# Performance work log

Hardware: AMD Instinct MI355X
Metric: run time of the kernel (lower is better)

The kernel has to match this reference:

```python
import jax, jax.numpy as jnp
import numpy as np

B, D, C, F = 1024, 8192, 345, 512
PROTO_W = 0.99  # args.proto_m


def setup_inputs() -> dict:
    key = jax.random.key(0)
    k = jax.random.split(key, 6)
    img_q = jax.random.normal(k[0], (B, D), jnp.float32)
    img_q1 = jax.random.normal(k[1], (B, D), jnp.float32)
    # partial label mask: random candidate set, guarantee >=1 candidate per row
    partial_Y = (jax.random.uniform(k[2], (B, C)) < 0.3).astype(jnp.float32)
    partial_Y = partial_Y.at[jnp.arange(B), jnp.arange(B) % C].set(1.0)
    W_enc = jax.random.normal(k[3], (D, F), jnp.float32) / np.sqrt(D).astype(np.float32)
    W_fc = jax.random.normal(k[4], (F, C), jnp.float32) / np.sqrt(F).astype(np.float32)
    b_fc = jnp.zeros((C,), jnp.float32)
    proto = jax.random.normal(k[5], (C, F), jnp.float32)
    proto = proto / jnp.linalg.norm(proto, axis=1, keepdims=True)
    return {"img_q": img_q, "img_q1": img_q1, "partial_Y": partial_Y,
            "W_enc": W_enc, "W_fc": W_fc, "b_fc": b_fc, "proto": proto}


def reference(img_q, img_q1, partial_Y, W_enc, W_fc, b_fc, proto):
    # encoder: feats [B,F], logits [B,C] (abstracted backbone + shared fc)
    feats_q = img_q @ W_enc
    logits_q = feats_q @ W_fc + b_fc
    feats_q1 = img_q1 @ W_enc
    logits_q1 = feats_q1 @ W_fc + b_fc

    # partial-label restricted pseudo labels
    scores = jax.nn.softmax(logits_q, axis=1) * partial_Y
    scores = scores / scores.sum(axis=1, keepdims=True)
    labels = jnp.argmax(scores, axis=1)  # [B] int

    # Sequential per-sample EMA p[l] = w*p[l] + (1-w)*f, vectorized in closed form.
    # For a sample with c_after same-label samples occurring later, its final
    # contribution is (1-w)*w^c_after * f; the old prototype is scaled by w^count.
    onehot = jax.nn.one_hot(labels, C, dtype=feats_q.dtype)   # [B,C]
    cum = jnp.cumsum(onehot, axis=0)                          # inclusive counts
    occ = cum[jnp.arange(B), labels] - 1.0                    # occurrences before i
    total = cum[-1]                                           # [C] per-class counts
    c_after = total[labels] - occ - 1.0                       # [B]
    coef = (1.0 - PROTO_W) * PROTO_W ** c_after               # [B]
    contrib = jax.ops.segment_sum(coef[:, None] * feats_q, labels, num_segments=C)
    new_proto = (PROTO_W ** total)[:, None] * proto + contrib
    new_proto = new_proto / jnp.linalg.norm(new_proto, axis=1, keepdims=True)

    prot_scores = new_proto @ W_fc + b_fc
    return logits_q, logits_q1, new_proto, prot_scores, labels, feats_q, feats_q1
```

## Files before the change

kernel.cpp:

```cpp
#include <hip/hip_runtime.h>
#include <float.h>
#include <math.h>

#define B_SZ 1024
#define D_SZ 8192
#define C_SZ 345
#define F_SZ 512
#define PROTO_W 0.99f


#define WS_XH 0
#define WS_XL 33554432u
#define WS_WH 67108864u
#define WS_WL 75497472u
#define WS_P  83886080u
#define WS2_WFH 100663296u
#define WS2_WFL 101056512u
#define WS2_LAB 101449728u
#define WS2_NEED 101457920u
#define WS2_FH 0u
#define WS2_FL 2097152u

#define WS_NEED 92274688u
#define WS_FH  0u
#define WS_FL  2097152u
#define WS_WFH 4194304u
#define WS_WFL 4587520u
#define WS_NPH 4980736u
#define WS_NPL 5373952u

typedef short bf16x8 __attribute__((ext_vector_type(8)));
typedef short short4v __attribute__((ext_vector_type(4)));
typedef short short8v __attribute__((ext_vector_type(8)));
typedef float f32x4  __attribute__((ext_vector_type(4)));

__device__ __forceinline__ void split_bf16(float x, short& hi, short& lo) {
    unsigned u = __float_as_uint(x);
    unsigned r = (u + 0x7FFFu + ((u >> 16) & 1u)) >> 16;
    hi = (short)r;
    float hf = __uint_as_float(r << 16);
    lo = (short)(__float_as_uint(x - hf) >> 16);
}
__device__ __forceinline__ float bf16_f32(short h) {
    return __uint_as_float(((unsigned)(unsigned short)h) << 16);
}

__device__ __forceinline__ void gl_lds16(const short* g, short* l) {
    __builtin_amdgcn_global_load_lds(
        (const __attribute__((address_space(1))) void*)g,
        (__attribute__((address_space(3))) void*)l, 16, 0, 0);
}

__device__ __forceinline__ unsigned f2key(float v) {
    unsigned u = __float_as_uint(v);
    return (u & 0x80000000u) ? ~u : (u | 0x80000000u);
}

__device__ __forceinline__ void fence_barrier() {
    asm volatile("" ::: "memory");
    __builtin_amdgcn_s_barrier();
    asm volatile("" ::: "memory");
}

#define MFMA_BF16 __builtin_amdgcn_mfma_f32_16x16x32_bf16

#define MFMA_BLOCK(IA0, IA1, IB0, IB1)                                   \
    do {                                                                 \
        bf16x8 a0h = *(const bf16x8*)&sAh[IA0];                          \
        bf16x8 a1h = *(const bf16x8*)&sAh[IA1];                          \
        bf16x8 b0h = *(const bf16x8*)&sBh[IB0];                          \
        bf16x8 b1h = *(const bf16x8*)&sBh[IB1];                          \
        bf16x8 a0l = *(const bf16x8*)&sAl[IA0];                          \
        bf16x8 a1l = *(const bf16x8*)&sAl[IA1];                          \
        bf16x8 b0l = *(const bf16x8*)&sBl[IB0];                          \
        bf16x8 b1l = *(const bf16x8*)&sBl[IB1];                          \
        acc[0][0] = MFMA_BF16(a0h, b0h, acc[0][0], 0, 0, 0);             \
        acc[0][1] = MFMA_BF16(a0h, b1h, acc[0][1], 0, 0, 0);             \
        acc[1][0] = MFMA_BF16(a1h, b0h, acc[1][0], 0, 0, 0);             \
        acc[1][1] = MFMA_BF16(a1h, b1h, acc[1][1], 0, 0, 0);             \
        acc[0][0] = MFMA_BF16(a0h, b0l, acc[0][0], 0, 0, 0);             \
        acc[0][1] = MFMA_BF16(a0h, b1l, acc[0][1], 0, 0, 0);             \
        acc[1][0] = MFMA_BF16(a1h, b0l, acc[1][0], 0, 0, 0);             \
        acc[1][1] = MFMA_BF16(a1h, b1l, acc[1][1], 0, 0, 0);             \
        acc[0][0] = MFMA_BF16(a0l, b0h, acc[0][0], 0, 0, 0);             \
        acc[0][1] = MFMA_BF16(a0l, b1h, acc[0][1], 0, 0, 0);             \
        acc[1][0] = MFMA_BF16(a1l, b0h, acc[1][0], 0, 0, 0);             \
        acc[1][1] = MFMA_BF16(a1l, b1h, acc[1][1], 0, 0, 0);             \
    } while (0)

__global__ __launch_bounds__(256) void convert_all(
    const float* __restrict__ img_q, const float* __restrict__ img_q1,
    const float* __restrict__ W_enc, const float* __restrict__ W_fc,
    short* __restrict__ Xh, short* __restrict__ Xl,
    short* __restrict__ Wh, short* __restrict__ Wl,
    short* __restrict__ Wth, short* __restrict__ Wtl)
{
    __shared__ float tile[64][65];
    const int bid = blockIdx.x;
    const int t = threadIdx.x;

    if (bid < 1024) {
        const int HALF = (B_SZ * D_SZ) / 4;
        const int total = 2 * HALF;
        for (int i4 = bid * 256 + t; i4 < total; i4 += 1024 * 256) {
            float4 v = (i4 < HALF) ? ((const float4*)img_q)[i4]
                                   : ((const float4*)img_q1)[i4 - HALF];
            short4v h, l;
            short hh, ll;
            split_bf16(v.x, hh, ll); h.x = hh; l.x = ll;
            split_bf16(v.y, hh, ll); h.y = hh; l.y = ll;
            split_bf16(v.z, hh, ll); h.z = hh; l.z = ll;
            split_bf16(v.w, hh, ll); h.w = hh; l.w = ll;
            ((short4v*)Xh)[i4] = h;
            ((short4v*)Xl)[i4] = l;
        }
    } else if (bid < 2048) {
        const int id = bid - 1024;
        const int k0 = (id >> 3) * 64;
        const int n0 = (id & 7) * 64;
        {
            const int kr = t >> 2;
            const int cb = (t & 3) * 16;
#pragma unroll
            for (int j = 0; j < 4; ++j) {
                float4 v = *(const float4*)&W_enc[(size_t)(k0 + kr) * F_SZ + n0 + cb + j * 4];
                tile[kr][cb + j * 4 + 0] = v.x;
                tile[kr][cb + j * 4 + 1] = v.y;
                tile[kr][cb + j * 4 + 2] = v.z;
                tile[kr][cb + j * 4 + 3] = v.w;
            }
        }
        __syncthreads();
        const int n = t >> 2;
#pragma unroll
        for (int cc = 0; cc < 2; ++cc) {
            const int ch = (t & 3) * 2 + cc;
            short8v h, l;
#pragma unroll
            for (int e = 0; e < 8; ++e) {
                short hh, ll;
                split_bf16(tile[ch * 8 + e][n], hh, ll);
                h[e] = hh; l[e] = ll;
            }
            size_t off = (size_t)(n0 + n) * D_SZ + k0 + ch * 8;
            *(short8v*)&Wh[off] = h;
            *(short8v*)&Wl[off] = l;
        }
    } else {
        const int id = bid - 2048;
        const int k0 = (id & 7) * 64;
        const int c0 = (id >> 3) * 64;
        for (int idx = t; idx < 64 * 64; idx += 256) {
            const int kr = idx >> 6;
            const int cc = idx & 63;
            tile[kr][cc] = (c0 + cc < C_SZ) ? W_fc[(size_t)(k0 + kr) * C_SZ + c0 + cc] : 0.0f;
        }
        __syncthreads();
        const int crow = t >> 2;
#pragma unroll
        for (int cc2 = 0; cc2 < 2; ++cc2) {
            const int ch = (t & 3) * 2 + cc2;
            short8v h, l;
#pragma unroll
            for (int e = 0; e < 8; ++e) {
                short hh, ll;
                split_bf16(tile[ch * 8 + e][crow], hh, ll);
                h[e] = hh; l[e] = ll;
            }
            size_t off = (size_t)(c0 + crow) * F_SZ + k0 + ch * 8;
            *(short8v*)&Wth[off] = h;
            *(short8v*)&Wtl[off] = l;
        }
    }
}

__global__ __launch_bounds__(512, 1) void gemm_ws128_v3(
    const short* __restrict__ Xh, const short* __restrict__ Xl,
    const short* __restrict__ Wh, const short* __restrict__ Wl,
    float* __restrict__ P, int ksteps)
{
    __shared__ __align__(16) short sAh[2][8192];
    __shared__ __align__(16) short sAl[2][8192];
    __shared__ __align__(16) short sBh[2][8192];
    __shared__ __align__(16) short sBl[2][8192];

    const int t = threadIdx.x;
    const int lane = t & 63;
    const int wave = t >> 6;

    const int flat = blockIdx.x + 4 * blockIdx.y + 64 * blockIdx.z;
    const int logical = (flat & 7) * 32 + (flat >> 3);
    const int nt = logical & 3;
    const int mt = (logical >> 2) & 15;
    const int ks = logical >> 6;

    const int m0 = mt * 128;
    const int n0 = nt * 128;
    const int kbase = ks * ksteps * 64;

    const int arr = wave >> 1;
    const int half = wave & 1;
    const short* gbase =
        (arr == 0) ? Xh + (size_t)m0 * D_SZ :
        (arr == 1) ? Xl + (size_t)m0 * D_SZ :
        (arr == 2) ? Wh + (size_t)n0 * D_SZ :
                     Wl + (size_t)n0 * D_SZ;
    short* lb[2];
    lb[0] = ((arr == 0) ? sAh[0] : (arr == 1) ? sAl[0] : (arr == 2) ? sBh[0] : sBl[0]) + half * 4096;
    lb[1] = ((arr == 0) ? sAh[1] : (arr == 1) ? sAl[1] : (arr == 2) ? sBh[1] : sBl[1]) + half * 4096;
    const int lrow8 = lane >> 3;
    const int gchunkOff = ((lane & 7) ^ lrow8) * 8;
    const short* gsrc = gbase + (size_t)(half * 64 + lrow8) * D_SZ + kbase + gchunkOff;

    const int wr = wave >> 2;
    const int wc = wave & 3;
    const int mo = wr * 64;
    const int no = wc * 32;
    const int lr = lane & 15;
    const int lkg = lane >> 4;
    const int x7 = lr & 7;
    const int sl0 = lkg ^ x7;
    const int sl1 = (4 + lkg) ^ x7;
    int aoff[4], boff[2];
#pragma unroll
    for (int f = 0; f < 4; ++f) aoff[f] = (mo + 16 * f + lr) * 64;
#pragma unroll
    for (int g = 0; g < 2; ++g) boff[g] = (no + 16 * g + lr) * 64;

    f32x4 acc[4][2] = {};

#pragma unroll
    for (int j = 0; j < 8; ++j)
        gl_lds16(gsrc + (size_t)(8 * j) * D_SZ, lb[0] + j * 512);

    int buf = 0;
    for (int s = 0; s < ksteps; ++s) {
        if (s + 1 < ksteps) {
            short* dst = lb[buf ^ 1];
            const short* g = gsrc + (s + 1) * 64;
#pragma unroll
            for (int j = 0; j < 8; ++j)
                gl_lds16(g + (size_t)(8 * j) * D_SZ, dst + j * 512);
            asm volatile("s_waitcnt vmcnt(8)" ::: "memory");
        } else {
            asm volatile("s_waitcnt vmcnt(0)" ::: "memory");
        }
        fence_barrier();

        const short* pAh = sAh[buf];
        const short* pAl = sAl[buf];
        const short* pBh = sBh[buf];
        const short* pBl = sBl[buf];

        {
            bf16x8 ah[4], al[4], bh[2], bl_[2];
#pragma unroll
            for (int f = 0; f < 4; ++f) {
                ah[f] = *(const bf16x8*)&pAh[aoff[f] + sl0 * 8];
                al[f] = *(const bf16x8*)&pAl[aoff[f] + sl0 * 8];
            }
#pragma unroll
            for (int g = 0; g < 2; ++g) {
                bh[g]  = *(const bf16x8*)&pBh[boff[g] + sl0 * 8];
                bl_[g] = *(const bf16x8*)&pBl[boff[g] + sl0 * 8];
            }
            __builtin_amdgcn_s_setprio(1);
#pragma unroll
            for (int f = 0; f < 4; ++f)
#pragma unroll
                for (int g = 0; g < 2; ++g)
                    acc[f][g] = MFMA_BF16(ah[f], bh[g], acc[f][g], 0, 0, 0);
#pragma unroll
            for (int f = 0; f < 4; ++f)
#pragma unroll
                for (int g = 0; g < 2; ++g)
                    acc[f][g] = MFMA_BF16(ah[f], bl_[g], acc[f][g], 0, 0, 0);
#pragma unroll
            for (int f = 0; f < 4; ++f)
#pragma unroll
                for (int g = 0; g < 2; ++g)
                    acc[f][g] = MFMA_BF16(al[f], bh[g], acc[f][g], 0, 0, 0);
            __builtin_amdgcn_s_setprio(0);
        }
        fence_barrier();

        {
            bf16x8 ah[4], al[4], bh[2], bl_[2];
#pragma unroll
            for (int f = 0; f < 4; ++f) {
                ah[f] = *(const bf16x8*)&pAh[aoff[f] + sl1 * 8];
                al[f] = *(const bf16x8*)&pAl[aoff[f] + sl1 * 8];
            }
#pragma unroll
            for (int g = 0; g < 2; ++g) {
                bh[g]  = *(const bf16x8*)&pBh[boff[g] + sl1 * 8];
                bl_[g] = *(const bf16x8*)&pBl[boff[g] + sl1 * 8];
            }
            __builtin_amdgcn_s_setprio(1);
#pragma unroll
            for (int f = 0; f < 4; ++f)
#pragma unroll
                for (int g = 0; g < 2; ++g)
                    acc[f][g] = MFMA_BF16(ah[f], bh[g], acc[f][g], 0, 0, 0);
#pragma unroll
            for (int f = 0; f < 4; ++f)
#pragma unroll
                for (int g = 0; g < 2; ++g)
                    acc[f][g] = MFMA_BF16(ah[f], bl_[g], acc[f][g], 0, 0, 0);
#pragma unroll
            for (int f = 0; f < 4; ++f)
#pragma unroll
                for (int g = 0; g < 2; ++g)
                    acc[f][g] = MFMA_BF16(al[f], bh[g], acc[f][g], 0, 0, 0);
            __builtin_amdgcn_s_setprio(0);
        }
        fence_barrier();
        buf ^= 1;
    }

    float* Pout = P + (size_t)ks * (2048u * 512u);
#pragma unroll
    for (int f = 0; f < 4; ++f)
#pragma unroll
        for (int g = 0; g < 2; ++g) {
            const int col  = n0 + no + 16 * g + (lane & 15);
            const int row0 = m0 + mo + 16 * f + (lane >> 4) * 4;
#pragma unroll
            for (int r = 0; r < 4; ++r)
                Pout[(size_t)(row0 + r) * F_SZ + col] = acc[f][g][r];
        }
}

__global__ __launch_bounds__(256, 1) void gemm_ws128(
    const short* __restrict__ Xh, const short* __restrict__ Xl,
    const short* __restrict__ Wh, const short* __restrict__ Wl,
    float* __restrict__ P, int ksteps)
{
    __shared__ __align__(16) short sAh[2][8192];
    __shared__ __align__(16) short sAl[2][8192];
    __shared__ __align__(16) short sBh[2][8192];
    __shared__ __align__(16) short sBl[2][8192];

    const int t = threadIdx.x;
    const int lane = t & 63;
    const int wave = t >> 6;
    const int nt = blockIdx.x;
    const int mt = blockIdx.y;
    const int ks = blockIdx.z;
    const int m0 = mt * 128;
    const int n0 = nt * 128;
    const int kbase = ks * ksteps * 64;

    const short* gbase =
        (wave == 0) ? Xh + (size_t)m0 * D_SZ :
        (wave == 1) ? Xl + (size_t)m0 * D_SZ :
        (wave == 2) ? Wh + (size_t)n0 * D_SZ :
                      Wl + (size_t)n0 * D_SZ;
    short* lb[2];
    lb[0] = (wave == 0) ? sAh[0] : (wave == 1) ? sAl[0] : (wave == 2) ? sBh[0] : sBl[0];
    lb[1] = (wave == 0) ? sAh[1] : (wave == 1) ? sAl[1] : (wave == 2) ? sBh[1] : sBl[1];
    const int lrow8 = lane >> 3;
    const int gchunkOff = ((lane & 7) ^ lrow8) * 8;
    const short* gsrc = gbase + (size_t)lrow8 * D_SZ + kbase + gchunkOff;

    const int mo = (wave >> 1) * 64;
    const int no = (wave & 1) * 64;
    const int lr = lane & 15;
    const int lkg = lane >> 4;
    const int x7 = lr & 7;
    const int sl0 = lkg ^ x7;
    const int sl1 = (4 + lkg) ^ x7;
    int aoff[4], boff[4];
#pragma unroll
    for (int f = 0; f < 4; ++f) {
        aoff[f] = (mo + 16 * f + lr) * 64;
        boff[f] = (no + 16 * f + lr) * 64;
    }

    f32x4 acc[4][4] = {};

#pragma unroll
    for (int j = 0; j < 16; ++j)
        gl_lds16(gsrc + (size_t)(8 * j) * D_SZ, lb[0] + j * 512);

    int buf = 0;
    for (int s = 0; s < ksteps; ++s) {
        if (s + 1 < ksteps) {
            short* dst = lb[buf ^ 1];
            const short* g = gsrc + (s + 1) * 64;
#pragma unroll
            for (int j = 0; j < 16; ++j)
                gl_lds16(g + (size_t)(8 * j) * D_SZ, dst + j * 512);
            asm volatile("s_waitcnt vmcnt(16)" ::: "memory");
        } else {
            asm volatile("s_waitcnt vmcnt(0)" ::: "memory");
        }
        fence_barrier();

        __builtin_amdgcn_s_setprio(1);
        {
            const short* pAh = sAh[buf];
            const short* pAl = sAl[buf];
            const short* pBh = sBh[buf];
            const short* pBl = sBl[buf];
#pragma unroll
            for (int ksub = 0; ksub < 2; ++ksub) {
                const int sl = ksub ? sl1 : sl0;
                bf16x8 ah[4], al[4], bh[4], blo[4];
#pragma unroll
                for (int f = 0; f < 4; ++f) {
                    ah[f]  = *(const bf16x8*)&pAh[aoff[f] + sl * 8];
                    al[f]  = *(const bf16x8*)&pAl[aoff[f] + sl * 8];
                }
#pragma unroll
                for (int g = 0; g < 4; ++g) {
                    bh[g]  = *(const bf16x8*)&pBh[boff[g] + sl * 8];
                    blo[g] = *(const bf16x8*)&pBl[boff[g] + sl * 8];
                }
#pragma unroll
                for (int f = 0; f < 4; ++f)
#pragma unroll
                    for (int g = 0; g < 4; ++g)
                        acc[f][g] = MFMA_BF16(ah[f], bh[g], acc[f][g], 0, 0, 0);
#pragma unroll
                for (int f = 0; f < 4; ++f)
#pragma unroll
                    for (int g = 0; g < 4; ++g)
                        acc[f][g] = MFMA_BF16(ah[f], blo[g], acc[f][g], 0, 0, 0);
#pragma unroll
                for (int f = 0; f < 4; ++f)
#pragma unroll
                    for (int g = 0; g < 4; ++g)
                        acc[f][g] = MFMA_BF16(al[f], bh[g], acc[f][g], 0, 0, 0);
            }
        }
        __builtin_amdgcn_s_setprio(0);
        fence_barrier();
        buf ^= 1;
    }

    float* Pout = P + (size_t)ks * (2048u * 512u);
#pragma unroll
    for (int f = 0; f < 4; ++f)
#pragma unroll
        for (int g = 0; g < 4; ++g) {
            const int col  = n0 + no + 16 * g + (lane & 15);
            const int row0 = m0 + mo + 16 * f + (lane >> 4) * 4;
#pragma unroll
            for (int r = 0; r < 4; ++r)
                Pout[(size_t)(row0 + r) * F_SZ + col] = acc[f][g][r];
        }
}

__global__ __launch_bounds__(256) void reduce_feats4(
    const float* __restrict__ P, float* __restrict__ feats,
    short* __restrict__ Fh, short* __restrict__ Fl)
{
    const int i4 = blockIdx.x * 256 + threadIdx.x;
    float4 a = ((const float4*)P)[i4];
#pragma unroll
    for (int sl = 1; sl < 4; ++sl) {
        float4 b = ((const float4*)(P + (size_t)sl * (2048u * 512u)))[i4];
        a.x += b.x; a.y += b.y; a.z += b.z; a.w += b.w;
    }
    ((float4*)feats)[i4] = a;
    float v[4] = {a.x, a.y, a.z, a.w};
    short4v h, l;
    short hh, ll;
#pragma unroll
    for (int e = 0; e < 4; ++e) {
        split_bf16(v[e], hh, ll); h[e] = hh; l[e] = ll;
    }
    ((short4v*)Fh)[i4] = h;
    ((short4v*)Fl)[i4] = l;
}

__global__ __launch_bounds__(256, 2) void fc_logits3(
    const short* __restrict__ Ah, const short* __restrict__ Al,
    const short* __restrict__ Bh_g, const short* __restrict__ Bl_g,
    const float* __restrict__ bias, const float* __restrict__ partial_Y,
    float* __restrict__ logits, unsigned long long* __restrict__ labPack)
{
    __shared__ __align__(16) short dAh[2][4096];
    __shared__ __align__(16) short dAl[2][4096];
    __shared__ __align__(16) short dBh[2][4096];
    __shared__ __align__(16) short dBl[2][4096];

    const int t = threadIdx.x;
    const int lane = t & 63;
    const int wave = t >> 6;
    const int n0 = blockIdx.x * 64;
    const int m0 = blockIdx.y * 64;

    const int lrow8 = lane >> 3;
    const int colOff = ((lane & 7) ^ lrow8) * 8;

    const short* gsrc = (wave == 0) ? Ah : (wave == 1) ? Al
                      : (wave == 2) ? Bh_g : Bl_g;
    const int rbase = (wave < 2) ? m0 : n0;
    short* lb[2];
    lb[0] = (wave == 0) ? dAh[0] : (wave == 1) ? dAl[0] : (wave == 2) ? dBh[0] : dBl[0];
    lb[1] = (wave == 0) ? dAh[1] : (wave == 1) ? dAl[1] : (wave == 2) ? dBh[1] : dBl[1];
    const short* gbase = gsrc + (size_t)(rbase + lrow8) * F_SZ + colOff;

    const int mo = (wave >> 1) * 32;
    const int no = (wave & 1) * 32;
    const int lr = lane & 15;
    const int lkg = lane >> 4;
    const int x7 = lr & 7;
    const int sl0 = (0 + lkg) ^ x7;
    const int sl1 = (4 + lkg) ^ x7;
    const int ra0 = (mo + lr) * 64,      ra1 = (mo + 16 + lr) * 64;
    const int rb0 = (no + lr) * 64,      rb1 = (no + 16 + lr) * 64;
    const int a00 = ra0 + sl0 * 8, a01 = ra0 + sl1 * 8;
    const int a10 = ra1 + sl0 * 8, a11 = ra1 + sl1 * 8;
    const int b00 = rb0 + sl0 * 8, b01 = rb0 + sl1 * 8;
    const int b10 = rb1 + sl0 * 8, b11 = rb1 + sl1 * 8;

    f32x4 acc[2][2] = {};

#pragma unroll
    for (int j = 0; j < 8; ++j)
        gl_lds16(gbase + (size_t)(8 * j) * F_SZ, lb[0] + j * 512);

    int buf = 0;
    for (int s = 0; s < 8; ++s) {
        if (s + 1 < 8) {
            short* dst = lb[buf ^ 1];
            const short* g = gbase + (s + 1) * 64;
#pragma unroll
            for (int j = 0; j < 8; ++j)
                gl_lds16(g + (size_t)(8 * j) * F_SZ, dst + j * 512);
            asm volatile("s_waitcnt vmcnt(8)" ::: "memory");
        } else {
            asm volatile("s_waitcnt vmcnt(0)" ::: "memory");
        }
        fence_barrier();
        __builtin_amdgcn_s_setprio(1);
        {
            const short* sAh = dAh[buf];
            const short* sAl = dAl[buf];
            const short* sBh = dBh[buf];
            const short* sBl = dBl[buf];
            MFMA_BLOCK(a00, a10, b00, b10);
            MFMA_BLOCK(a01, a11, b01, b11);
        }
        __builtin_amdgcn_s_setprio(0);
        fence_barrier();
        buf ^= 1;
    }

    const bool doArg = (m0 < B_SZ);
#pragma unroll
    for (int f = 0; f < 2; ++f) {
#pragma unroll
        for (int r = 0; r < 4; ++r) {
            const int row = m0 + mo + f * 16 + (lane >> 4) * 4 + r;
            unsigned long long best = 0;
#pragma unroll
            for (int g = 0; g < 2; ++g) {
                const int col = n0 + no + g * 16 + (lane & 15);
                if (col < C_SZ) {
                    const float v = acc[f][g][r] + bias[col];
                    logits[(size_t)row * C_SZ + col] = v;
                    if (doArg && partial_Y[(size_t)row * C_SZ + col] != 0.0f) {
                        unsigned long long p = ((unsigned long long)f2key(v) << 32)
                                             | (unsigned long long)(0xFFFFFFFFu - (unsigned)col);
                        if (p > best) best = p;
                    }
                }
            }
            if (doArg) {
#pragma unroll
                for (int m = 1; m < 16; m <<= 1) {
                    unsigned long long o = __shfl_xor(best, m);
                    if (o > best) best = o;
                }
                if ((lane & 15) == 0 && best != 0)
                    atomicMax(&labPack[row], best);
            }
        }
    }
}

__global__ __launch_bounds__(512) void proto_scores_fused(
    const unsigned long long* __restrict__ labPack,
    const float* __restrict__ feats_q,
    const float* __restrict__ proto,
    const short* __restrict__ Wth, const short* __restrict__ Wtl,
    const float* __restrict__ b_fc,
    float* __restrict__ new_proto, float* __restrict__ scores,
    float* __restrict__ labels_f)
{
    __shared__ int rowlist[B_SZ];
    __shared__ int mcount_s;
    __shared__ float nprow[F_SZ];
    __shared__ float red[8];
    __shared__ float rinv_s;
    const int c = blockIdx.x;
    const int t = threadIdx.x;
    const int lane = t & 63;
    const int w = t >> 6;

    if (c == 0) {
#pragma unroll
        for (int j = 0; j < 2; ++j) {
            const int i = t + j * 512;
            int li = (int)(0xFFFFFFFFu - (unsigned)(labPack[i] & 0xFFFFFFFFull));
            labels_f[i] = (float)li;
        }
    }

    if (w == 0) {
        int k = 0;
#pragma unroll
        for (int ch = 0; ch < 16; ++ch) {
            unsigned long long pk = labPack[ch * 64 + lane];
            int li = (int)(0xFFFFFFFFu - (unsigned)(pk & 0xFFFFFFFFull));
            unsigned long long mask = __ballot(li == c);
            if (lane == 0) {
                while (mask) {
                    int p = __builtin_ctzll(mask);
                    mask &= mask - 1;
                    rowlist[k++] = ch * 64 + p;
                }
            }
            k = __shfl(k, 0);
        }
        if (lane == 0) mcount_s = k;
    }
    __syncthreads();
    const int m = mcount_s;

    float val = proto[(size_t)c * F_SZ + t];
    for (int k = 0; k < m; ++k)
        val = PROTO_W * val + (1.0f - PROTO_W) * feats_q[(size_t)rowlist[k] * F_SZ + t];

    float sq = val * val;
#pragma unroll
    for (int off = 32; off; off >>= 1) sq += __shfl_down(sq, off);
    if ((t & 63) == 0) red[t >> 6] = sq;
    __syncthreads();
    if (t == 0) {
        float s = 0.0f;
#pragma unroll
        for (int ww = 0; ww < 8; ++ww) s += red[ww];
        rinv_s = 1.0f / sqrtf(s);
    }
    __syncthreads();
    const float v = val * rinv_s;
    new_proto[(size_t)c * F_SZ + t] = v;
    nprow[t] = v;
    __syncthreads();

    float np8[8];
#pragma unroll
    for (int j = 0; j < 8; ++j) np8[j] = nprow[lane * 8 + j];
    for (int col = w; col < C_SZ; col += 8) {
        const short8v h = *(const short8v*)&Wth[(size_t)col * F_SZ + lane * 8];
        const short8v l = *(const short8v*)&Wtl[(size_t)col * F_SZ + lane * 8];
        float p = 0.0f;
#pragma unroll
        for (int j = 0; j < 8; ++j)
            p += np8[j] * (bf16_f32(h[j]) + bf16_f32(l[j]));
#pragma unroll
        for (int off = 32; off; off >>= 1) p += __shfl_down(p, off);
        if (lane == 0) scores[(size_t)c * C_SZ + col] = p + b_fc[col];
    }
}

__global__ __launch_bounds__(256) void reduce_feats_split(
    const float* __restrict__ P, float* __restrict__ feats,
    short* __restrict__ Fh, short* __restrict__ Fl,
    const float* __restrict__ W_fc,
    short* __restrict__ Wth, short* __restrict__ Wtl)
{
    const int bid = blockIdx.x;
    const int t = threadIdx.x;
    if (bid < 1024) {
        const int n4 = (2048 * 512) / 4;
        const float* P1 = P + 2048 * 512;
        for (int i4 = bid * 256 + t; i4 < n4; i4 += 1024 * 256) {
            float4 a = ((const float4*)P)[i4];
            float4 b = ((const float4*)P1)[i4];
            float v[4] = {a.x + b.x, a.y + b.y, a.z + b.z, a.w + b.w};
            short4v h, l;
            short hh, ll;
#pragma unroll
            for (int e = 0; e < 4; ++e) {
                feats[i4 * 4 + e] = v[e];
                split_bf16(v[e], hh, ll); h[e] = hh; l[e] = ll;
            }
            ((short4v*)Fh)[i4] = h;
            ((short4v*)Fl)[i4] = l;
        }
    } else {
        __shared__ float tile[64][65];
        const int id = bid - 1024;
        const int k0 = (id & 7) * 64;
        const int c0 = (id >> 3) * 64;
        for (int idx = t; idx < 64 * 64; idx += 256) {
            const int kr = idx >> 6;
            const int cc = idx & 63;
            tile[kr][cc] = (c0 + cc < C_SZ) ? W_fc[(size_t)(k0 + kr) * C_SZ + c0 + cc] : 0.0f;
        }
        __syncthreads();
        const int crow = t >> 2;
#pragma unroll
        for (int cc2 = 0; cc2 < 2; ++cc2) {
            const int ch = (t & 3) * 2 + cc2;
            short8v h, l;
#pragma unroll
            for (int e = 0; e < 8; ++e) {
                short hh, ll;
                split_bf16(tile[ch * 8 + e][crow], hh, ll);
                h[e] = hh; l[e] = ll;
            }
            size_t off = (size_t)(c0 + crow) * F_SZ + k0 + ch * 8;
            *(short8v*)&Wth[off] = h;
            *(short8v*)&Wtl[off] = l;
        }
    }
}

__global__ __launch_bounds__(256) void gemm_fc(
    const short* __restrict__ Ah, const short* __restrict__ Al,
    const short* __restrict__ Bh, const short* __restrict__ Bl,
    const float* __restrict__ bias, float* __restrict__ Cout, int M)
{
    __shared__ __align__(16) short sAh[4096];
    __shared__ __align__(16) short sAl[4096];
    __shared__ __align__(16) short sBh[4096];
    __shared__ __align__(16) short sBl[4096];

    const int t = threadIdx.x;
    const int lane = t & 63;
    const int wave = t >> 6;
    const int n0 = blockIdx.x * 64;
    const int m0 = blockIdx.y * 64;

    const int lrow8 = lane >> 3;
    const int colOff = ((lane & 7) ^ lrow8) * 8;

    short* lbase = (wave == 0) ? sAh : (wave == 1) ? sAl : (wave == 2) ? sBh : sBl;
    const short* gA = (wave == 1) ? Al : Ah;
    const short* gB = (wave == 3) ? Bl : Bh;
    const bool isA = wave < 2;

    const int mo = (wave >> 1) * 32;
    const int no = (wave & 1) * 32;
    const int lr = lane & 15;
    const int lkg = lane >> 4;
    const int x7 = lr & 7;
    const int sl0 = (0 + lkg) ^ x7;
    const int sl1 = (4 + lkg) ^ x7;
    const int ra0 = (mo + lr) * 64,      ra1 = (mo + 16 + lr) * 64;
    const int rb0 = (no + lr) * 64,      rb1 = (no + 16 + lr) * 64;
    const int a00 = ra0 + sl0 * 8, a01 = ra0 + sl1 * 8;
    const int a10 = ra1 + sl0 * 8, a11 = ra1 + sl1 * 8;
    const int b00 = rb0 + sl0 * 8, b01 = rb0 + sl1 * 8;
    const int b10 = rb1 + sl0 * 8, b11 = rb1 + sl1 * 8;

    f32x4 acc[2][2] = {};

    for (int s = 0; s < 8; ++s) {
        __syncthreads();
        if (isA) {
#pragma unroll
            for (int j = 0; j < 8; ++j) {
                int row = m0 + lrow8 + 8 * j;
                if (row > M - 1) row = M - 1;
                gl_lds16(gA + (size_t)row * F_SZ + s * 64 + colOff, lbase + j * 512);
            }
        } else {
#pragma unroll
            for (int j = 0; j < 8; ++j) {
                int row = n0 + lrow8 + 8 * j;
                gl_lds16(gB + (size_t)row * F_SZ + s * 64 + colOff, lbase + j * 512);
            }
        }
        __syncthreads();
        MFMA_BLOCK(a00, a10, b00, b10);
        MFMA_BLOCK(a01, a11, b01, b11);
    }

#pragma unroll
    for (int f = 0; f < 2; ++f)
#pragma unroll
        for (int g = 0; g < 2; ++g) {
            const int col  = n0 + no + g * 16 + (lane & 15);
            if (col >= C_SZ) continue;
            const float bb = bias[col];
            const int row0 = m0 + mo + f * 16 + (lane >> 4) * 4;
#pragma unroll
            for (int r = 0; r < 4; ++r) {
                const int row = row0 + r;
                if (row < M)
                    Cout[(size_t)row * C_SZ + col] = acc[f][g][r] + bb;
            }
        }
}

__global__ __launch_bounds__(64) void argmax_labels(
    const float* __restrict__ logits, const float* __restrict__ partial_Y,
    float* __restrict__ labels_f)
{
    const int i = blockIdx.x;
    const int lane = threadIdx.x;
    float best = -FLT_MAX;
    int bidx = C_SZ;
    for (int c = lane; c < C_SZ; c += 64) {
        if (partial_Y[(size_t)i * C_SZ + c] != 0.0f) {
            float v = logits[(size_t)i * C_SZ + c];
            if (v > best || (v == best && c < bidx)) { best = v; bidx = c; }
        }
    }
#pragma unroll
    for (int off = 32; off; off >>= 1) {
        float ov = __shfl_down(best, off);
        int oi = __shfl_down(bidx, off);
        if (ov > best || (ov == best && oi < bidx)) { best = ov; bidx = oi; }
    }
    if (lane == 0) labels_f[i] = (float)bidx;
}

__global__ __launch_bounds__(512) void proto_update(
    const float* __restrict__ labels_f, const float* __restrict__ feats_q,
    const float* __restrict__ proto, float* __restrict__ new_proto,
    short* __restrict__ NPh, short* __restrict__ NPl)
{
    __shared__ int lab[B_SZ];
    __shared__ float red[8];
    __shared__ float rinv_s;
    const int c = blockIdx.x;
    const int t = threadIdx.x;
    for (int i = t; i < B_SZ; i += 512) lab[i] = (int)labels_f[i];
    __syncthreads();
    float val = proto[(size_t)c * F_SZ + t];
    for (int i = 0; i < B_SZ; ++i) {
        if (lab[i] == c)
            val = PROTO_W * val + (1.0f - PROTO_W) * feats_q[(size_t)i * F_SZ + t];
    }
    float sq = val * val;
#pragma unroll
    for (int off = 32; off; off >>= 1) sq += __shfl_down(sq, off);
    if ((t & 63) == 0) red[t >> 6] = sq;
    __syncthreads();
    if (t == 0) {
        float s = 0.0f;
#pragma unroll
        for (int w = 0; w < 8; ++w) s += red[w];
        rinv_s = 1.0f / sqrtf(s);
    }
    __syncthreads();
    const float v = val * rinv_s;
    new_proto[(size_t)c * F_SZ + t] = v;
    if (NPh) {
        short hh, ll;
        split_bf16(v, hh, ll);
        NPh[(size_t)c * F_SZ + t] = hh;
        NPl[(size_t)c * F_SZ + t] = ll;
    }
}

extern "C" void kernel_launch(void* const* d_in, const int* in_sizes, int n_in,
                              void* d_out, int out_size, void* d_ws, size_t ws_size,
                              hipStream_t stream)
{
    const float* img_q     = (const float*)d_in[0];
    const float* img_q1    = (const float*)d_in[1];
    const float* partial_Y = (const float*)d_in[2];
    const float* W_enc     = (const float*)d_in[3];
    const float* W_fc      = (const float*)d_in[4];
    const float* b_fc      = (const float*)d_in[5];
    const float* proto     = (const float*)d_in[6];

    float* out       = (float*)d_out;
    float* logits    = out;
    float* new_proto = out + 706560;
    float* scores    = out + 883200;
    float* labels_f  = out + 1002225;
    float* feats     = out + 1003249;

    char* ws = (char*)d_ws;
    short* Xh = (short*)(ws + WS_XH);
    short* Xl = (short*)(ws + WS_XL);
    short* Wh = (short*)(ws + WS_WH);
    short* Wl = (short*)(ws + WS_WL);
    float* P  = (float*)(ws + WS_P);

    if (ws_size >= (size_t)WS2_NEED) {
        short* Wth = (short*)(ws + WS2_WFH);
        short* Wtl = (short*)(ws + WS2_WFL);
        unsigned long long* labPack = (unsigned long long*)(ws + WS2_LAB);
        short* Fh = (short*)(ws + WS2_FH);
        short* Fl = (short*)(ws + WS2_FL);

        hipMemsetAsync(labPack, 0, B_SZ * sizeof(unsigned long long), stream);
        hipLaunchKernelGGL(convert_all, dim3(2096), dim3(256), 0, stream,
                           img_q, img_q1, W_enc, W_fc, Xh, Xl, Wh, Wl, Wth, Wtl);
        hipLaunchKernelGGL(gemm_ws128_v3, dim3(4, 16, 4), dim3(512), 0, stream,
                           Xh, Xl, Wh, Wl, P, 32);
        hipLaunchKernelGGL(reduce_feats4, dim3(1024), dim3(256), 0, stream,
                           P, feats, Fh, Fl);
        hipLaunchKernelGGL(fc_logits3, dim3(6, 32), dim3(256), 0, stream,
                           Fh, Fl, Wth, Wtl, b_fc, partial_Y, logits, labPack);
        hipLaunchKernelGGL(proto_scores_fused, dim3(345), dim3(512), 0, stream,
                           labPack, feats, proto, Wth, Wtl, b_fc,
                           new_proto, scores, labels_f);
    } else {
        short* Fh  = (short*)(ws + WS_FH);
        short* Fl  = (short*)(ws + WS_FL);
        short* Wth = (short*)(ws + WS_WFH);
        short* Wtl = (short*)(ws + WS_WFL);
        short* NPh = (short*)(ws + WS_NPH);
        short* NPl = (short*)(ws + WS_NPL);

        hipLaunchKernelGGL(convert_all, dim3(2048), dim3(256), 0, stream,
                           img_q, img_q1, W_enc, W_fc, Xh, Xl, Wh, Wl,
                           (short*)nullptr, (short*)nullptr);
        hipLaunchKernelGGL(gemm_ws128, dim3(4, 16, 2), dim3(256), 0, stream,
                           Xh, Xl, Wh, Wl, P, 64);
        hipLaunchKernelGGL(reduce_feats_split, dim3(1072), dim3(256), 0, stream,
                           P, feats, Fh, Fl, W_fc, Wth, Wtl);
        hipLaunchKernelGGL(gemm_fc, dim3(6, 32), dim3(256), 0, stream,
                           Fh, Fl, Wth, Wtl, b_fc, logits, 2048);
        hipLaunchKernelGGL(argmax_labels, dim3(1024), dim3(64), 0, stream,
                           logits, partial_Y, labels_f);
        hipLaunchKernelGGL(proto_update, dim3(345), dim3(512), 0, stream,
                           labels_f, feats, proto, new_proto, NPh, NPl);
        hipLaunchKernelGGL(gemm_fc, dim3(6, 6), dim3(256), 0, stream,
                           NPh, NPl, Wth, Wtl, b_fc, scores, C_SZ);
    }
}
```

Measured before the change: 248.2 us.

## Pre-pack bf16 split operands into tile-contiguous swizzled layout for GEMM

The conversion kernel now writes the hi/lo bf16 splits of the inputs and the encoder weight into a per-tile, per-kstep packed layout that already matches the swizzled LDS layout. This lets the main GEMM load each k-step as one contiguous 16 KB chunk instead of strided rows. The labPack clear is folded into the conversion kernel, which drops a separate memset launch. The cost is a more scattered write pattern during conversion, including a transposed store path for W_enc.

```diff
diff --git a/kernel.cpp b/kernel.cpp
--- a/kernel.cpp
+++ b/kernel.cpp
@@ -18,8 +18,6 @@
 #define WS2_WFL 101056512u
 #define WS2_LAB 101449728u
 #define WS2_NEED 101457920u
-#define WS2_FH 0u
-#define WS2_FL 2097152u
 
 #define WS_NEED 92274688u
 #define WS_FH  0u
@@ -88,16 +86,505 @@
         acc[1][1] = MFMA_BF16(a1l, b1h, acc[1][1], 0, 0, 0);             \
     } while (0)
 
+__device__ __forceinline__ int packed_off(int r, int c) {
+    const int half = r >> 6;
+    const int rh = r & 63;
+    const int j = rh >> 3;
+    const int r8 = rh & 7;
+    const int l = (r8 << 3) | (c ^ r8);
+    return half * 4096 + j * 512 + l * 8;
+}
+
+__global__ __launch_bounds__(256) void convert_pack(
+    const float* __restrict__ img_q, const float* __restrict__ img_q1,
+    const float* __restrict__ W_enc, const float* __restrict__ W_fc,
+    short* __restrict__ Ahp, short* __restrict__ Alp,
+    short* __restrict__ Bhp, short* __restrict__ Blp,
+    short* __restrict__ Wth, short* __restrict__ Wtl,
+    unsigned long long* __restrict__ labPack)
+{
+    __shared__ float tile[64][65];
+    const int bid = blockIdx.x;
+    const int t = threadIdx.x;
+
+    if (bid < 4)
+        labPack[bid * 256 + t] = 0ull;
+
+    if (bid < 1024) {
+        const int total = 2048 * 1024;
+        for (int i = bid * 256 + t; i < total; i += 1024 * 256) {
+            const int row = i >> 10;
+            const int cc = i & 1023;
+            const float* src = (row < B_SZ)
+                ? &img_q[(size_t)row * D_SZ + cc * 8]
+                : &img_q1[(size_t)(row - B_SZ) * D_SZ + cc * 8];
+            float4 a = ((const float4*)src)[0];
+            float4 b = ((const float4*)src)[1];
+            float f[8] = {a.x, a.y, a.z, a.w, b.x, b.y, b.z, b.w};
+            short8v h, l;
+#pragma unroll
+            for (int e = 0; e < 8; ++e) {
+                short hh, ll;
+                split_bf16(f[e], hh, ll);
+                h[e] = hh; l[e] = ll;
+            }
+            const int mt = row >> 7;
+            const int pr = row & 127;
+            const int kstep = cc >> 3;
+            const int c = cc & 7;
+            const size_t dst = (size_t)(mt * 128 + kstep) * 8192 + packed_off(pr, c);
+            *(short8v*)&Ahp[dst] = h;
+            *(short8v*)&Alp[dst] = l;
+        }
+    } else if (bid < 2048) {
+        const int id = bid - 1024;
+        const int kstep = id >> 3;
+        const int k0 = kstep * 64;
+        const int n0 = (id & 7) * 64;
+        {
+            const int kr = t >> 2;
+            const int cb = (t & 3) * 16;
+#pragma unroll
+            for (int j = 0; j < 4; ++j) {
+                float4 v = *(const float4*)&W_enc[(size_t)(k0 + kr) * F_SZ + n0 + cb + j * 4];
+                tile[kr][cb + j * 4 + 0] = v.x;
+                tile[kr][cb + j * 4 + 1] = v.y;
+                tile[kr][cb + j * 4 + 2] = v.z;
+                tile[kr][cb + j * 4 + 3] = v.w;
+            }
+        }
+        __syncthreads();
+        const int n = t >> 2;
+#pragma unroll
+        for (int cc2 = 0; cc2 < 2; ++cc2) {
+            const int ch = (t & 3) * 2 + cc2;
+            short8v h, l;
+#pragma unroll
+            for (int e = 0; e < 8; ++e) {
+                short hh, ll;
+                split_bf16(tile[ch * 8 + e][n], hh, ll);
+                h[e] = hh; l[e] = ll;
+            }
+            const int nrow = n0 + n;
+            const int nt = nrow >> 7;
+            const int pr = nrow & 127;
+            const size_t dst = (size_t)(nt * 128 + kstep) * 8192 + packed_off(pr, ch);
+            *(short8v*)&Bhp[dst] = h;
+            *(short8v*)&Blp[dst] = l;
+        }
+    } else {
+        const int id = bid - 2048;
+        const int k0 = (id & 7) * 64;
+        const int c0 = (id >> 3) * 64;
+        for (int idx = t; idx < 64 * 64; idx += 256) {
+            const int kr = idx >> 6;
+            const int cc = idx & 63;
+            tile[kr][cc] = (c0 + cc < C_SZ) ? W_fc[(size_t)(k0 + kr) * C_SZ + c0 + cc] : 0.0f;
+        }
+        __syncthreads();
+        const int crow = t >> 2;
+#pragma unroll
+        for (int cc2 = 0; cc2 < 2; ++cc2) {
+            const int ch = (t & 3) * 2 + cc2;
+            short8v h, l;
+#pragma unroll
+            for (int e = 0; e < 8; ++e) {
+                short hh, ll;
+                split_bf16(tile[ch * 8 + e][crow], hh, ll);
+                h[e] = hh; l[e] = ll;
+            }
+            size_t off = (size_t)(c0 + crow) * F_SZ + k0 + ch * 8;
+            *(short8v*)&Wth[off] = h;
+            *(short8v*)&Wtl[off] = l;
+        }
+    }
+}
+
+__global__ __launch_bounds__(512, 1) void gemm_ws128_v4(
+    const short* __restrict__ Ahp, const short* __restrict__ Alp,
+    const short* __restrict__ Bhp, const short* __restrict__ Blp,
+    float* __restrict__ P, int ksteps)
+{
+    __shared__ __align__(16) short sAh[2][8192];
+    __shared__ __align__(16) short sAl[2][8192];
+    __shared__ __align__(16) short sBh[2][8192];
+    __shared__ __align__(16) short sBl[2][8192];
+
+    const int t = threadIdx.x;
+    const int lane = t & 63;
+    const int wave = t >> 6;
+
+    const int flat = blockIdx.x + 4 * blockIdx.y + 64 * blockIdx.z;
+    const int logical = (flat & 7) * 32 + (flat >> 3);
+    const int nt = logical & 3;
+    const int mt = (logical >> 2) & 15;
+    const int ks = logical >> 6;
+
+    const int m0 = mt * 128;
+    const int n0 = nt * 128;
+
+    const int arr = wave >> 1;
+    const int half = wave & 1;
+    const short* gtile =
+        (arr == 0) ? Ahp + (size_t)(mt * 128) * 8192 :
+        (arr == 1) ? Alp + (size_t)(mt * 128) * 8192 :
+        (arr == 2) ? Bhp + (size_t)(nt * 128) * 8192 :
+                     Blp + (size_t)(nt * 128) * 8192;
+    short* lb[2];
+    lb[0] = ((arr == 0) ? sAh[0] : (arr == 1) ? sAl[0] : (arr == 2) ? sBh[0] : sBl[0]) + half * 4096;
+    lb[1] = ((arr == 0) ? sAh[1] : (arr == 1) ? sAl[1] : (arr == 2) ? sBh[1] : sBl[1]) + half * 4096;
+    const short* gsrc0 = gtile + (size_t)(ks * ksteps) * 8192 + half * 4096 + lane * 8;
+
+    const int wr = wave >> 2;
+    const int wc = wave & 3;
+    const int mo = wr * 64;
+    const int no = wc * 32;
+    const int lr = lane & 15;
+    const int lkg = lane >> 4;
+    const int x7 = lr & 7;
+    const int sl0 = lkg ^ x7;
+    const int sl1 = (4 + lkg) ^ x7;
+    int aoff[4], boff[2];
+#pragma unroll
+    for (int f = 0; f < 4; ++f) aoff[f] = (mo + 16 * f + lr) * 64;
+#pragma unroll
+    for (int g = 0; g < 2; ++g) boff[g] = (no + 16 * g + lr) * 64;
+
+    f32x4 acc[4][2] = {};
+
+#pragma unroll
+    for (int j = 0; j < 8; ++j)
+        gl_lds16(gsrc0 + j * 512, lb[0] + j * 512);
+
+    int buf = 0;
+    for (int s = 0; s < ksteps; ++s) {
+        if (s + 1 < ksteps) {
+            short* dst = lb[buf ^ 1];
+            const short* g = gsrc0 + (size_t)(s + 1) * 8192;
+#pragma unroll
+            for (int j = 0; j < 8; ++j)
+                gl_lds16(g + j * 512, dst + j * 512);
+            asm volatile("s_waitcnt vmcnt(8)" ::: "memory");
+        } else {
+            asm volatile("s_waitcnt vmcnt(0)" ::: "memory");
+        }
+        fence_barrier();
+
+        const short* pAh = sAh[buf];
+        const short* pAl = sAl[buf];
+        const short* pBh = sBh[buf];
+        const short* pBl = sBl[buf];
+
+        {
+            bf16x8 ah[4], al[4], bh[2], bl_[2];
+#pragma unroll
+            for (int f = 0; f < 4; ++f) {
+                ah[f] = *(const bf16x8*)&pAh[aoff[f] + sl0 * 8];
+                al[f] = *(const bf16x8*)&pAl[aoff[f] + sl0 * 8];
+            }
+#pragma unroll
+            for (int g = 0; g < 2; ++g) {
+                bh[g]  = *(const bf16x8*)&pBh[boff[g] + sl0 * 8];
+                bl_[g] = *(const bf16x8*)&pBl[boff[g] + sl0 * 8];
+            }
+            __builtin_amdgcn_s_setprio(1);
+#pragma unroll
+            for (int f = 0; f < 4; ++f)
+#pragma unroll
+                for (int g = 0; g < 2; ++g)
+                    acc[f][g] = MFMA_BF16(ah[f], bh[g], acc[f][g], 0, 0, 0);
+#pragma unroll
+            for (int f = 0; f < 4; ++f)
+#pragma unroll
+                for (int g = 0; g < 2; ++g)
+                    acc[f][g] = MFMA_BF16(ah[f], bl_[g], acc[f][g], 0, 0, 0);
+#pragma unroll
+            for (int f = 0; f < 4; ++f)
+#pragma unroll
+                for (int g = 0; g < 2; ++g)
+                    acc[f][g] = MFMA_BF16(al[f], bh[g], acc[f][g], 0, 0, 0);
+            __builtin_amdgcn_s_setprio(0);
+        }
+        fence_barrier();
+
+        {
+            bf16x8 ah[4], al[4], bh[2], bl_[2];
+#pragma unroll
+            for (int f = 0; f < 4; ++f) {
+                ah[f] = *(const bf16x8*)&pAh[aoff[f] + sl1 * 8];
+                al[f] = *(const bf16x8*)&pAl[aoff[f] + sl1 * 8];
+            }
+#pragma unroll
+            for (int g = 0; g < 2; ++g) {
+                bh[g]  = *(const bf16x8*)&pBh[boff[g] + sl1 * 8];
+                bl_[g] = *(const bf16x8*)&pBl[boff[g] + sl1 * 8];
+            }
+            __builtin_amdgcn_s_setprio(1);
+#pragma unroll
+            for (int f = 0; f < 4; ++f)
+#pragma unroll
+                for (int g = 0; g < 2; ++g)
+                    acc[f][g] = MFMA_BF16(ah[f], bh[g], acc[f][g], 0, 0, 0);
+#pragma unroll
+            for (int f = 0; f < 4; ++f)
+#pragma unroll
+                for (int g = 0; g < 2; ++g)
+                    acc[f][g] = MFMA_BF16(ah[f], bl_[g], acc[f][g], 0, 0, 0);
+#pragma unroll
+            for (int f = 0; f < 4; ++f)
+#pragma unroll
+                for (int g = 0; g < 2; ++g)
+                    acc[f][g] = MFMA_BF16(al[f], bh[g], acc[f][g], 0, 0, 0);
+            __builtin_amdgcn_s_setprio(0);
+        }
+        fence_barrier();
+        buf ^= 1;
+    }
+
+    float* Pout = P + (size_t)ks * (2048u * 512u);
+#pragma unroll
+    for (int f = 0; f < 4; ++f)
+#pragma unroll
+        for (int g = 0; g < 2; ++g) {
+            const int col  = n0 + no + 16 * g + (lane & 15);
+            const int row0 = m0 + mo + 16 * f + (lane >> 4) * 4;
+#pragma unroll
+            for (int r = 0; r < 4; ++r)
+                Pout[(size_t)(row0 + r) * F_SZ + col] = acc[f][g][r];
+        }
+}
+
+__global__ __launch_bounds__(256) void reduce_feats4(
+    const float* __restrict__ P, float* __restrict__ feats,
+    short* __restrict__ Fh, short* __restrict__ Fl)
+{
+    const int i4 = blockIdx.x * 256 + threadIdx.x;
+    float4 a = ((const float4*)P)[i4];
+#pragma unroll
+    for (int sl = 1; sl < 4; ++sl) {
+        float4 b = ((const float4*)(P + (size_t)sl * (2048u * 512u)))[i4];
+        a.x += b.x; a.y += b.y; a.z += b.z; a.w += b.w;
+    }
+    ((float4*)feats)[i4] = a;
+    float v[4] = {a.x, a.y, a.z, a.w};
+    short4v h, l;
+    short hh, ll;
+#pragma unroll
+    for (int e = 0; e < 4; ++e) {
+        split_bf16(v[e], hh, ll); h[e] = hh; l[e] = ll;
+    }
+    ((short4v*)Fh)[i4] = h;
+    ((short4v*)Fl)[i4] = l;
+}
+
+__global__ __launch_bounds__(256, 2) void fc_logits3(
+    const short* __restrict__ Ah, const short* __restrict__ Al,
+    const short* __restrict__ Bh_g, const short* __restrict__ Bl_g,
+    const float* __restrict__ bias, const float* __restrict__ partial_Y,
+    float* __restrict__ logits, unsigned long long* __restrict__ labPack)
+{
+    __shared__ __align__(16) short dAh[2][4096];
+    __shared__ __align__(16) short dAl[2][4096];
+    __shared__ __align__(16) short dBh[2][4096];
+    __shared__ __align__(16) short dBl[2][4096];
+
+    const int t = threadIdx.x;
+    const int lane = t & 63;
+    const int wave = t >> 6;
+    const int n0 = blockIdx.x * 64;
+    const int m0 = blockIdx.y * 64;
+
+    const int lrow8 = lane >> 3;
+    const int colOff = ((lane & 7) ^ lrow8) * 8;
+
+    const short* gsrc = (wave == 0) ? Ah : (wave == 1) ? Al
+                      : (wave == 2) ? Bh_g : Bl_g;
+    const int rbase = (wave < 2) ? m0 : n0;
+    short* lb[2];
+    lb[0] = (wave == 0) ? dAh[0] : (wave == 1) ? dAl[0] : (wave == 2) ? dBh[0] : dBl[0];
+    lb[1] = (wave == 0) ? dAh[1] : (wave == 1) ? dAl[1] : (wave == 2) ? dBh[1] : dBl[1];
+    const short* gbase = gsrc + (size_t)(rbase + lrow8) * F_SZ + colOff;
+
+    const int mo = (wave >> 1) * 32;
+    const int no = (wave & 1) * 32;
+    const int lr = lane & 15;
+    const int lkg = lane >> 4;
+    const int x7 = lr & 7;
+    const int sl0 = (0 + lkg) ^ x7;
+    const int sl1 = (4 + lkg) ^ x7;
+    const int ra0 = (mo + lr) * 64,      ra1 = (mo + 16 + lr) * 64;
+    const int rb0 = (no + lr) * 64,      rb1 = (no + 16 + lr) * 64;
+    const int a00 = ra0 + sl0 * 8, a01 = ra0 + sl1 * 8;
+    const int a10 = ra1 + sl0 * 8, a11 = ra1 + sl1 * 8;
+    const int b00 = rb0 + sl0 * 8, b01 = rb0 + sl1 * 8;
+    const int b10 = rb1 + sl0 * 8, b11 = rb1 + sl1 * 8;
+
+    f32x4 acc[2][2] = {};
+
+#pragma unroll
+    for (int j = 0; j < 8; ++j)
+        gl_lds16(gbase + (size_t)(8 * j) * F_SZ, lb[0] + j * 512);
+
+    int buf = 0;
+    for (int s = 0; s < 8; ++s) {
+        if (s + 1 < 8) {
+            short* dst = lb[buf ^ 1];
+            const short* g = gbase + (s + 1) * 64;
+#pragma unroll
+            for (int j = 0; j < 8; ++j)
+                gl_lds16(g + (size_t)(8 * j) * F_SZ, dst + j * 512);
+            asm volatile("s_waitcnt vmcnt(8)" ::: "memory");
+        } else {
+            asm volatile("s_waitcnt vmcnt(0)" ::: "memory");
+        }
+        fence_barrier();
+        __builtin_amdgcn_s_setprio(1);
+        {
+            const short* sAh = dAh[buf];
+            const short* sAl = dAl[buf];
+            const short* sBh = dBh[buf];
+            const short* sBl = dBl[buf];
+            MFMA_BLOCK(a00, a10, b00, b10);
+            MFMA_BLOCK(a01, a11, b01, b11);
+        }
+        __builtin_amdgcn_s_setprio(0);
+        fence_barrier();
+        buf ^= 1;
+    }
+
+    const bool doArg = (m0 < B_SZ);
+#pragma unroll
+    for (int f = 0; f < 2; ++f) {
+#pragma unroll
+        for (int r = 0; r < 4; ++r) {
+            const int row = m0 + mo + f * 16 + (lane >> 4) * 4 + r;
+            unsigned long long best = 0;
+#pragma unroll
+            for (int g = 0; g < 2; ++g) {
+                const int col = n0 + no + g * 16 + (lane & 15);
+                if (col < C_SZ) {
+                    const float v = acc[f][g][r] + bias[col];
+                    logits[(size_t)row * C_SZ + col] = v;
+                    if (doArg && partial_Y[(size_t)row * C_SZ + col] != 0.0f) {
+                        unsigned long long p = ((unsigned long long)f2key(v) << 32)
+                                             | (unsigned long long)(0xFFFFFFFFu - (unsigned)col);
+                        if (p > best) best = p;
+                    }
+                }
+            }
+            if (doArg) {
+#pragma unroll
+                for (int m = 1; m < 16; m <<= 1) {
+                    unsigned long long o = __shfl_xor(best, m);
+                    if (o > best) best = o;
+                }
+                if ((lane & 15) == 0 && best != 0)
+                    atomicMax(&labPack[row], best);
+            }
+        }
+    }
+}
+
+__global__ __launch_bounds__(512) void proto_scores_fused(
+    const unsigned long long* __restrict__ labPack,
+    const float* __restrict__ feats_q,
+    const float* __restrict__ proto,
+    const short* __restrict__ Wth, const short* __restrict__ Wtl,
+    const float* __restrict__ b_fc,
+    float* __restrict__ new_proto, float* __restrict__ scores,
+    float* __restrict__ labels_f)
+{
+    __shared__ int rowlist[B_SZ];
+    __shared__ int mcount_s;
+    __shared__ float nprow[F_SZ];
+    __shared__ float red[8];
+    __shared__ float rinv_s;
+    const int c = blockIdx.x;
+    const int t = threadIdx.x;
+    const int lane = t & 63;
+    const int w = t >> 6;
+
+    if (c == 0) {
+#pragma unroll
+        for (int j = 0; j < 2; ++j) {
+            const int i = t + j * 512;
+            int li = (int)(0xFFFFFFFFu - (unsigned)(labPack[i] & 0xFFFFFFFFull));
+            labels_f[i] = (float)li;
+        }
+    }
+
+    if (w == 0) {
+        int k = 0;
+#pragma unroll
+        for (int ch = 0; ch < 16; ++ch) {
+            unsigned long long pk = labPack[ch * 64 + lane];
+            int li = (int)(0xFFFFFFFFu - (unsigned)(pk & 0xFFFFFFFFull));
+            unsigned long long mask = __ballot(li == c);
+            if (lane == 0) {
+                while (mask) {
+                    int p = __builtin_ctzll(mask);
+                    mask &= mask - 1;
+                    rowlist[k++] = ch * 64 + p;
+                }
+            }
+            k = __shfl(k, 0);
+        }
+        if (lane == 0) mcount_s = k;
+    }
+    __syncthreads();
+    const int m = mcount_s;
+
+    float val = proto[(size_t)c * F_SZ + t];
+    for (int k = 0; k < m; ++k)
+        val = PROTO_W * val + (1.0f - PROTO_W) * feats_q[(size_t)rowlist[k] * F_SZ + t];
+
+    float sq = val * val;
+#pragma unroll
+    for (int off = 32; off; off >>= 1) sq += __shfl_down(sq, off);
+    if ((t & 63) == 0) red[t >> 6] = sq;
+    __syncthreads();
+    if (t == 0) {
+        float s = 0.0f;
+#pragma unroll
+        for (int ww = 0; ww < 8; ++ww) s += red[ww];
+        rinv_s = 1.0f / sqrtf(s);
+    }
+    __syncthreads();
+    const float v = val * rinv_s;
+    new_proto[(size_t)c * F_SZ + t] = v;
+    nprow[t] = v;
+    __syncthreads();
+
+    float np8[8];
+#pragma unroll
+    for (int j = 0; j < 8; ++j) np8[j] = nprow[lane * 8 + j];
+    for (int col = w; col < C_SZ; col += 8) {
+        const short8v h = *(const short8v*)&Wth[(size_t)col * F_SZ + lane * 8];
+        const short8v l = *(const short8v*)&Wtl[(size_t)col * F_SZ + lane * 8];
+        float p = 0.0f;
+#pragma unroll
+        for (int j = 0; j < 8; ++j)
+            p += np8[j] * (bf16_f32(h[j]) + bf16_f32(l[j]));
+#pragma unroll
+        for (int off = 32; off; off >>= 1) p += __shfl_down(p, off);
+        if (lane == 0) scores[(size_t)c * C_SZ + col] = p + b_fc[col];
+    }
+}
+
 __global__ __launch_bounds__(256) void convert_all(
     const float* __restrict__ img_q, const float* __restrict__ img_q1,
     const float* __restrict__ W_enc, const float* __restrict__ W_fc,
     short* __restrict__ Xh, short* __restrict__ Xl,
     short* __restrict__ Wh, short* __restrict__ Wl,
-    short* __restrict__ Wth, short* __restrict__ Wtl)
+    short* __restrict__ Wth, short* __restrict__ Wtl,
+    unsigned long long* __restrict__ labPack)
 {
     __shared__ float tile[64][65];
     const int bid = blockIdx.x;
     const int t = threadIdx.x;
+
+    if (labPack && bid < 4)
+        labPack[bid * 256 + t] = 0ull;
 
     if (bid < 1024) {
         const int HALF = (B_SZ * D_SZ) / 4;
@@ -174,163 +661,6 @@
     }
 }
 
-__global__ __launch_bounds__(512, 1) void gemm_ws128_v3(
-    const short* __restrict__ Xh, const short* __restrict__ Xl,
-    const short* __restrict__ Wh, const short* __restrict__ Wl,
-    float* __restrict__ P, int ksteps)
-{
-    __shared__ __align__(16) short sAh[2][8192];
-    __shared__ __align__(16) short sAl[2][8192];
-    __shared__ __align__(16) short sBh[2][8192];
-    __shared__ __align__(16) short sBl[2][8192];
-
-    const int t = threadIdx.x;
-    const int lane = t & 63;
-    const int wave = t >> 6;
-
-    const int flat = blockIdx.x + 4 * blockIdx.y + 64 * blockIdx.z;
-    const int logical = (flat & 7) * 32 + (flat >> 3);
-    const int nt = logical & 3;
-    const int mt = (logical >> 2) & 15;
-    const int ks = logical >> 6;
-
-    const int m0 = mt * 128;
-    const int n0 = nt * 128;
-    const int kbase = ks * ksteps * 64;
-
-    const int arr = wave >> 1;
-    const int half = wave & 1;
-    const short* gbase =
-        (arr == 0) ? Xh + (size_t)m0 * D_SZ :
-        (arr == 1) ? Xl + (size_t)m0 * D_SZ :
-        (arr == 2) ? Wh + (size_t)n0 * D_SZ :
-                     Wl + (size_t)n0 * D_SZ;
-    short* lb[2];
-    lb[0] = ((arr == 0) ? sAh[0] : (arr == 1) ? sAl[0] : (arr == 2) ? sBh[0] : sBl[0]) + half * 4096;
-    lb[1] = ((arr == 0) ? sAh[1] : (arr == 1) ? sAl[1] : (arr == 2) ? sBh[1] : sBl[1]) + half * 4096;
-    const int lrow8 = lane >> 3;
-    const int gchunkOff = ((lane & 7) ^ lrow8) * 8;
-    const short* gsrc = gbase + (size_t)(half * 64 + lrow8) * D_SZ + kbase + gchunkOff;
-
-    const int wr = wave >> 2;
-    const int wc = wave & 3;
-    const int mo = wr * 64;
-    const int no = wc * 32;
-    const int lr = lane & 15;
-    const int lkg = lane >> 4;
-    const int x7 = lr & 7;
-    const int sl0 = lkg ^ x7;
-    const int sl1 = (4 + lkg) ^ x7;
-    int aoff[4], boff[2];
-#pragma unroll
-    for (int f = 0; f < 4; ++f) aoff[f] = (mo + 16 * f + lr) * 64;
-#pragma unroll
-    for (int g = 0; g < 2; ++g) boff[g] = (no + 16 * g + lr) * 64;
-
-    f32x4 acc[4][2] = {};
-
-#pragma unroll
-    for (int j = 0; j < 8; ++j)
-        gl_lds16(gsrc + (size_t)(8 * j) * D_SZ, lb[0] + j * 512);
-
-    int buf = 0;
-    for (int s = 0; s < ksteps; ++s) {
-        if (s + 1 < ksteps) {
-            short* dst = lb[buf ^ 1];
-            const short* g = gsrc + (s + 1) * 64;
-#pragma unroll
-            for (int j = 0; j < 8; ++j)
-                gl_lds16(g + (size_t)(8 * j) * D_SZ, dst + j * 512);
-            asm volatile("s_waitcnt vmcnt(8)" ::: "memory");
-        } else {
-            asm volatile("s_waitcnt vmcnt(0)" ::: "memory");
-        }
-        fence_barrier();
-
-        const short* pAh = sAh[buf];
-        const short* pAl = sAl[buf];
-        const short* pBh = sBh[buf];
-        const short* pBl = sBl[buf];
-
-        {
-            bf16x8 ah[4], al[4], bh[2], bl_[2];
-#pragma unroll
-            for (int f = 0; f < 4; ++f) {
-                ah[f] = *(const bf16x8*)&pAh[aoff[f] + sl0 * 8];
-                al[f] = *(const bf16x8*)&pAl[aoff[f] + sl0 * 8];
-            }
-#pragma unroll
-            for (int g = 0; g < 2; ++g) {
-                bh[g]  = *(const bf16x8*)&pBh[boff[g] + sl0 * 8];
-                bl_[g] = *(const bf16x8*)&pBl[boff[g] + sl0 * 8];
-            }
-            __builtin_amdgcn_s_setprio(1);
-#pragma unroll
-            for (int f = 0; f < 4; ++f)
-#pragma unroll
-                for (int g = 0; g < 2; ++g)
-                    acc[f][g] = MFMA_BF16(ah[f], bh[g], acc[f][g], 0, 0, 0);
-#pragma unroll
-            for (int f = 0; f < 4; ++f)
-#pragma unroll
-                for (int g = 0; g < 2; ++g)
-                    acc[f][g] = MFMA_BF16(ah[f], bl_[g], acc[f][g], 0, 0, 0);
-#pragma unroll
-            for (int f = 0; f < 4; ++f)
-#pragma unroll
-                for (int g = 0; g < 2; ++g)
-                    acc[f][g] = MFMA_BF16(al[f], bh[g], acc[f][g], 0, 0, 0);
-            __builtin_amdgcn_s_setprio(0);
-        }
-        fence_barrier();
-
-        {
-            bf16x8 ah[4], al[4], bh[2], bl_[2];
-#pragma unroll
-            for (int f = 0; f < 4; ++f) {
-                ah[f] = *(const bf16x8*)&pAh[aoff[f] + sl1 * 8];
-                al[f] = *(const bf16x8*)&pAl[aoff[f] + sl1 * 8];
-            }
-#pragma unroll
-            for (int g = 0; g < 2; ++g) {
-                bh[g]  = *(const bf16x8*)&pBh[boff[g] + sl1 * 8];
-                bl_[g] = *(const bf16x8*)&pBl[boff[g] + sl1 * 8];
-            }
-            __builtin_amdgcn_s_setprio(1);
-#pragma unroll
-            for (int f = 0; f < 4; ++f)
-#pragma unroll
-                for (int g = 0; g < 2; ++g)
-                    acc[f][g] = MFMA_BF16(ah[f], bh[g], acc[f][g], 0, 0, 0);
-#pragma unroll
-            for (int f = 0; f < 4; ++f)
-#pragma unroll
-                for (int g = 0; g < 2; ++g)
-                    acc[f][g] = MFMA_BF16(ah[f], bl_[g], acc[f][g], 0, 0, 0);
-#pragma unroll
-            for (int f = 0; f < 4; ++f)
-#pragma unroll
-                for (int g = 0; g < 2; ++g)
-                    acc[f][g] = MFMA_BF16(al[f], bh[g], acc[f][g], 0, 0, 0);
-            __builtin_amdgcn_s_setprio(0);
-        }
-        fence_barrier();
-        buf ^= 1;
-    }
-
-    float* Pout = P + (size_t)ks * (2048u * 512u);
-#pragma unroll
-    for (int f = 0; f < 4; ++f)
-#pragma unroll
-        for (int g = 0; g < 2; ++g) {
-            const int col  = n0 + no + 16 * g + (lane & 15);
-            const int row0 = m0 + mo + 16 * f + (lane >> 4) * 4;
-#pragma unroll
-            for (int r = 0; r < 4; ++r)
-                Pout[(size_t)(row0 + r) * F_SZ + col] = acc[f][g][r];
-        }
-}
-
 __global__ __launch_bounds__(256, 1) void gemm_ws128(
     const short* __restrict__ Xh, const short* __restrict__ Xl,
     const short* __restrict__ Wh, const short* __restrict__ Wl,
@@ -452,39 +782,69 @@
         }
 }
 
-__global__ __launch_bounds__(256) void reduce_feats4(
+__global__ __launch_bounds__(256) void reduce_feats_split(
     const float* __restrict__ P, float* __restrict__ feats,
-    short* __restrict__ Fh, short* __restrict__ Fl)
-{
-    const int i4 = blockIdx.x * 256 + threadIdx.x;
-    float4 a = ((const float4*)P)[i4];
-#pragma unroll
-    for (int sl = 1; sl < 4; ++sl) {
-        float4 b = ((const float4*)(P + (size_t)sl * (2048u * 512u)))[i4];
-        a.x += b.x; a.y += b.y; a.z += b.z; a.w += b.w;
-    }
-    ((float4*)feats)[i4] = a;
-    float v[4] = {a.x, a.y, a.z, a.w};
-    short4v h, l;
-    short hh, ll;
-#pragma unroll
-    for (int e = 0; e < 4; ++e) {
-        split_bf16(v[e], hh, ll); h[e] = hh; l[e] = ll;
-    }
-    ((short4v*)Fh)[i4] = h;
-    ((short4v*)Fl)[i4] = l;
-}
-
-__global__ __launch_bounds__(256, 2) void fc_logits3(
+    short* __restrict__ Fh, short* __restrict__ Fl,
+    const float* __restrict__ W_fc,
+    short* __restrict__ Wth, short* __restrict__ Wtl)
+{
+    const int bid = blockIdx.x;
+    const int t = threadIdx.x;
+    if (bid < 1024) {
+        const int n4 = (2048 * 512) / 4;
+        const float* P1 = P + 2048 * 512;
+        for (int i4 = bid * 256 + t; i4 < n4; i4 += 1024 * 256) {
+            float4 a = ((const float4*)P)[i4];
+            float4 b = ((const float4*)P1)[i4];
+            float v[4] = {a.x + b.x, a.y + b.y, a.z + b.z, a.w + b.w};
+            short4v h, l;
+            short hh, ll;
+#pragma unroll
+            for (int e = 0; e < 4; ++e) {
+                feats[i4 * 4 + e] = v[e];
+                split_bf16(v[e], hh, ll); h[e] = hh; l[e] = ll;
+            }
+            ((short4v*)Fh)[i4] = h;
+            ((short4v*)Fl)[i4] = l;
+        }
+    } else {
+        __shared__ float tile[64][65];
+        const int id = bid - 1024;
+        const int k0 = (id & 7) * 64;
+        const int c0 = (id >> 3) * 64;
+        for (int idx = t; idx < 64 * 64; idx += 256) {
+            const int kr = idx >> 6;
+            const int cc = idx & 63;
+            tile[kr][cc] = (c0 + cc < C_SZ) ? W_fc[(size_t)(k0 + kr) * C_SZ + c0 + cc] : 0.0f;
+        }
+        __syncthreads();
+        const int crow = t >> 2;
+#pragma unroll
+        for (int cc2 = 0; cc2 < 2; ++cc2) {
+            const int ch = (t & 3) * 2 + cc2;
+            short8v h, l;
+#pragma unroll
+            for (int e = 0; e < 8; ++e) {
+                short hh, ll;
+                split_bf16(tile[ch * 8 + e][crow], hh, ll);
+                h[e] = hh; l[e] = ll;
+            }
+            size_t off = (size_t)(c0 + crow) * F_SZ + k0 + ch * 8;
+            *(short8v*)&Wth[off] = h;
+            *(short8v*)&Wtl[off] = l;
+        }
+    }
+}
+
+__global__ __launch_bounds__(256) void gemm_fc(
     const short* __restrict__ Ah, const short* __restrict__ Al,
-    const short* __restrict__ Bh_g, const short* __restrict__ Bl_g,
-    const float* __restrict__ bias, const float* __restrict__ partial_Y,
-    float* __restrict__ logits, unsigned long long* __restrict__ labPack)
-{
-    __shared__ __align__(16) short dAh[2][4096];
-    __shared__ __align__(16) short dAl[2][4096];
-    __shared__ __align__(16) short dBh[2][4096];
-    __shared__ __align__(16) short dBl[2][4096];
+    const short* __restrict__ Bh, const short* __restrict__ Bl,
+    const float* __restrict__ bias, float* __restrict__ Cout, int M)
+{
+    __shared__ __align__(16) short sAh[4096];
+    __shared__ __align__(16) short sAl[4096];
+    __shared__ __align__(16) short sBh[4096];
+    __shared__ __align__(16) short sBl[4096];
 
     const int t = threadIdx.x;
     const int lane = t & 63;
@@ -495,13 +855,10 @@
     const int lrow8 = lane >> 3;
     const int colOff = ((lane & 7) ^ lrow8) * 8;
 
-    const short* gsrc = (wave == 0) ? Ah : (wave == 1) ? Al
-                      : (wave == 2) ? Bh_g : Bl_g;
-    const int rbase = (wave < 2) ? m0 : n0;
-    short* lb[2];
-    lb[0] = (wave == 0) ? dAh[0] : (wave == 1) ? dAl[0] : (wave == 2) ? dBh[0] : dBl[0];
-    lb[1] = (wave == 0) ? dAh[1] : (wave == 1) ? dAl[1] : (wave == 2) ? dBh[1] : dBl[1];
-    const short* gbase = gsrc + (size_t)(rbase + lrow8) * F_SZ + colOff;
+    short* lbase = (wave == 0) ? sAh : (wave == 1) ? sAl : (wave == 2) ? sBh : sBl;
+    const short* gA = (wave == 1) ? Al : Ah;
+    const short* gB = (wave == 3) ? Bl : Bh;
+    const bool isA = wave < 2;
 
     const int mo = (wave >> 1) * 32;
     const int no = (wave & 1) * 32;
@@ -519,250 +876,6 @@
 
     f32x4 acc[2][2] = {};
 
-#pragma unroll
-    for (int j = 0; j < 8; ++j)
-        gl_lds16(gbase + (size_t)(8 * j) * F_SZ, lb[0] + j * 512);
-
-    int buf = 0;
-    for (int s = 0; s < 8; ++s) {
-        if (s + 1 < 8) {
-            short* dst = lb[buf ^ 1];
-            const short* g = gbase + (s + 1) * 64;
-#pragma unroll
-            for (int j = 0; j < 8; ++j)
-                gl_lds16(g + (size_t)(8 * j) * F_SZ, dst + j * 512);
-            asm volatile("s_waitcnt vmcnt(8)" ::: "memory");
-        } else {
-            asm volatile("s_waitcnt vmcnt(0)" ::: "memory");
-        }
-        fence_barrier();
-        __builtin_amdgcn_s_setprio(1);
-        {
-            const short* sAh = dAh[buf];
-            const short* sAl = dAl[buf];
-            const short* sBh = dBh[buf];
-            const short* sBl = dBl[buf];
-            MFMA_BLOCK(a00, a10, b00, b10);
-            MFMA_BLOCK(a01, a11, b01, b11);
-        }
-        __builtin_amdgcn_s_setprio(0);
-        fence_barrier();
-        buf ^= 1;
-    }
-
-    const bool doArg = (m0 < B_SZ);
-#pragma unroll
-    for (int f = 0; f < 2; ++f) {
-#pragma unroll
-        for (int r = 0; r < 4; ++r) {
-            const int row = m0 + mo + f * 16 + (lane >> 4) * 4 + r;
-            unsigned long long best = 0;
-#pragma unroll
-            for (int g = 0; g < 2; ++g) {
-                const int col = n0 + no + g * 16 + (lane & 15);
-                if (col < C_SZ) {
-                    const float v = acc[f][g][r] + bias[col];
-                    logits[(size_t)row * C_SZ + col] = v;
-                    if (doArg && partial_Y[(size_t)row * C_SZ + col] != 0.0f) {
-                        unsigned long long p = ((unsigned long long)f2key(v) << 32)
-                                             | (unsigned long long)(0xFFFFFFFFu - (unsigned)col);
-                        if (p > best) best = p;
-                    }
-                }
-            }
-            if (doArg) {
-#pragma unroll
-                for (int m = 1; m < 16; m <<= 1) {
-                    unsigned long long o = __shfl_xor(best, m);
-                    if (o > best) best = o;
-                }
-                if ((lane & 15) == 0 && best != 0)
-                    atomicMax(&labPack[row], best);
-            }
-        }
-    }
-}
-
-__global__ __launch_bounds__(512) void proto_scores_fused(
-    const unsigned long long* __restrict__ labPack,
-    const float* __restrict__ feats_q,
-    const float* __restrict__ proto,
-    const short* __restrict__ Wth, const short* __restrict__ Wtl,
-    const float* __restrict__ b_fc,
-    float* __restrict__ new_proto, float* __restrict__ scores,
-    float* __restrict__ labels_f)
-{
-    __shared__ int rowlist[B_SZ];
-    __shared__ int mcount_s;
-    __shared__ float nprow[F_SZ];
-    __shared__ float red[8];
-    __shared__ float rinv_s;
-    const int c = blockIdx.x;
-    const int t = threadIdx.x;
-    const int lane = t & 63;
-    const int w = t >> 6;
-
-    if (c == 0) {
-#pragma unroll
-        for (int j = 0; j < 2; ++j) {
-            const int i = t + j * 512;
-            int li = (int)(0xFFFFFFFFu - (unsigned)(labPack[i] & 0xFFFFFFFFull));
-            labels_f[i] = (float)li;
-        }
-    }
-
-    if (w == 0) {
-        int k = 0;
-#pragma unroll
-        for (int ch = 0; ch < 16; ++ch) {
-            unsigned long long pk = labPack[ch * 64 + lane];
-            int li = (int)(0xFFFFFFFFu - (unsigned)(pk & 0xFFFFFFFFull));
-            unsigned long long mask = __ballot(li == c);
-            if (lane == 0) {
-                while (mask) {
-                    int p = __builtin_ctzll(mask);
-                    mask &= mask - 1;
-                    rowlist[k++] = ch * 64 + p;
-                }
-            }
-            k = __shfl(k, 0);
-        }
-        if (lane == 0) mcount_s = k;
-    }
-    __syncthreads();
-    const int m = mcount_s;
-
-    float val = proto[(size_t)c * F_SZ + t];
-    for (int k = 0; k < m; ++k)
-        val = PROTO_W * val + (1.0f - PROTO_W) * feats_q[(size_t)rowlist[k] * F_SZ + t];
-
-    float sq = val * val;
-#pragma unroll
-    for (int off = 32; off; off >>= 1) sq += __shfl_down(sq, off);
-    if ((t & 63) == 0) red[t >> 6] = sq;
-    __syncthreads();
-    if (t == 0) {
-        float s = 0.0f;
-#pragma unroll
-        for (int ww = 0; ww < 8; ++ww) s += red[ww];
-        rinv_s = 1.0f / sqrtf(s);
-    }
-    __syncthreads();
-    const float v = val * rinv_s;
-    new_proto[(size_t)c * F_SZ + t] = v;
-    nprow[t] = v;
-    __syncthreads();
-
-    float np8[8];
-#pragma unroll
-    for (int j = 0; j < 8; ++j) np8[j] = nprow[lane * 8 + j];
-    for (int col = w; col < C_SZ; col += 8) {
-        const short8v h = *(const short8v*)&Wth[(size_t)col * F_SZ + lane * 8];
-        const short8v l = *(const short8v*)&Wtl[(size_t)col * F_SZ + lane * 8];
-        float p = 0.0f;
-#pragma unroll
-        for (int j = 0; j < 8; ++j)
-            p += np8[j] * (bf16_f32(h[j]) + bf16_f32(l[j]));
-#pragma unroll
-        for (int off = 32; off; off >>= 1) p += __shfl_down(p, off);
-        if (lane == 0) scores[(size_t)c * C_SZ + col] = p + b_fc[col];
-    }
-}
-
-__global__ __launch_bounds__(256) void reduce_feats_split(
-    const float* __restrict__ P, float* __restrict__ feats,
-    short* __restrict__ Fh, short* __restrict__ Fl,
-    const float* __restrict__ W_fc,
-    short* __restrict__ Wth, short* __restrict__ Wtl)
-{
-    const int bid = blockIdx.x;
-    const int t = threadIdx.x;
-    if (bid < 1024) {
-        const int n4 = (2048 * 512) / 4;
-        const float* P1 = P + 2048 * 512;
-        for (int i4 = bid * 256 + t; i4 < n4; i4 += 1024 * 256) {
-            float4 a = ((const float4*)P)[i4];
-            float4 b = ((const float4*)P1)[i4];
-            float v[4] = {a.x + b.x, a.y + b.y, a.z + b.z, a.w + b.w};
-            short4v h, l;
-            short hh, ll;
-#pragma unroll
-            for (int e = 0; e < 4; ++e) {
-                feats[i4 * 4 + e] = v[e];
-                split_bf16(v[e], hh, ll); h[e] = hh; l[e] = ll;
-            }
-            ((short4v*)Fh)[i4] = h;
-            ((short4v*)Fl)[i4] = l;
-        }
-    } else {
-        __shared__ float tile[64][65];
-        const int id = bid - 1024;
-        const int k0 = (id & 7) * 64;
-        const int c0 = (id >> 3) * 64;
-        for (int idx = t; idx < 64 * 64; idx += 256) {
-            const int kr = idx >> 6;
-            const int cc = idx & 63;
-            tile[kr][cc] = (c0 + cc < C_SZ) ? W_fc[(size_t)(k0 + kr) * C_SZ + c0 + cc] : 0.0f;
-        }
-        __syncthreads();
-        const int crow = t >> 2;
-#pragma unroll
-        for (int cc2 = 0; cc2 < 2; ++cc2) {
-            const int ch = (t & 3) * 2 + cc2;
-            short8v h, l;
-#pragma unroll
-            for (int e = 0; e < 8; ++e) {
-                short hh, ll;
-                split_bf16(tile[ch * 8 + e][crow], hh, ll);
-                h[e] = hh; l[e] = ll;
-            }
-            size_t off = (size_t)(c0 + crow) * F_SZ + k0 + ch * 8;
-            *(short8v*)&Wth[off] = h;
-            *(short8v*)&Wtl[off] = l;
-        }
-    }
-}
-
-__global__ __launch_bounds__(256) void gemm_fc(
-    const short* __restrict__ Ah, const short* __restrict__ Al,
-    const short* __restrict__ Bh, const short* __restrict__ Bl,
-    const float* __restrict__ bias, float* __restrict__ Cout, int M)
-{
-    __shared__ __align__(16) short sAh[4096];
-    __shared__ __align__(16) short sAl[4096];
-    __shared__ __align__(16) short sBh[4096];
-    __shared__ __align__(16) short sBl[4096];
-
-    const int t = threadIdx.x;
-    const int lane = t & 63;
-    const int wave = t >> 6;
-    const int n0 = blockIdx.x * 64;
-    const int m0 = blockIdx.y * 64;
-
-    const int lrow8 = lane >> 3;
-    const int colOff = ((lane & 7) ^ lrow8) * 8;
-
-    short* lbase = (wave == 0) ? sAh : (wave == 1) ? sAl : (wave == 2) ? sBh : sBl;
-    const short* gA = (wave == 1) ? Al : Ah;
-    const short* gB = (wave == 3) ? Bl : Bh;
-    const bool isA = wave < 2;
-
-    const int mo = (wave >> 1) * 32;
-    const int no = (wave & 1) * 32;
-    const int lr = lane & 15;
-    const int lkg = lane >> 4;
-    const int x7 = lr & 7;
-    const int sl0 = (0 + lkg) ^ x7;
-    const int sl1 = (4 + lkg) ^ x7;
-    const int ra0 = (mo + lr) * 64,      ra1 = (mo + 16 + lr) * 64;
-    const int rb0 = (no + lr) * 64,      rb1 = (no + 16 + lr) * 64;
-    const int a00 = ra0 + sl0 * 8, a01 = ra0 + sl1 * 8;
-    const int a10 = ra1 + sl0 * 8, a11 = ra1 + sl1 * 8;
-    const int b00 = rb0 + sl0 * 8, b01 = rb0 + sl1 * 8;
-    const int b10 = rb1 + sl0 * 8, b11 = rb1 + sl1 * 8;
-
-    f32x4 acc[2][2] = {};
-
     for (int s = 0; s < 8; ++s) {
         __syncthreads();
         if (isA) {
@@ -893,13 +1006,13 @@
         short* Wth = (short*)(ws + WS2_WFH);
         short* Wtl = (short*)(ws + WS2_WFL);
         unsigned long long* labPack = (unsigned long long*)(ws + WS2_LAB);
-        short* Fh = (short*)(ws + WS2_FH);
-        short* Fl = (short*)(ws + WS2_FL);
-
-        hipMemsetAsync(labPack, 0, B_SZ * sizeof(unsigned long long), stream);
-        hipLaunchKernelGGL(convert_all, dim3(2096), dim3(256), 0, stream,
-                           img_q, img_q1, W_enc, W_fc, Xh, Xl, Wh, Wl, Wth, Wtl);
-        hipLaunchKernelGGL(gemm_ws128_v3, dim3(4, 16, 4), dim3(512), 0, stream,
+        short* Fh = (short*)(ws + 0u);
+        short* Fl = (short*)(ws + 2097152u);
+
+        hipLaunchKernelGGL(convert_pack, dim3(2096), dim3(256), 0, stream,
+                           img_q, img_q1, W_enc, W_fc, Xh, Xl, Wh, Wl, Wth, Wtl,
+                           labPack);
+        hipLaunchKernelGGL(gemm_ws128_v4, dim3(4, 16, 4), dim3(512), 0, stream,
                            Xh, Xl, Wh, Wl, P, 32);
         hipLaunchKernelGGL(reduce_feats4, dim3(1024), dim3(256), 0, stream,
                            P, feats, Fh, Fl);
@@ -918,7 +1031,8 @@
 
         hipLaunchKernelGGL(convert_all, dim3(2048), dim3(256), 0, stream,
                            img_q, img_q1, W_enc, W_fc, Xh, Xl, Wh, Wl,
-                           (short*)nullptr, (short*)nullptr);
+                           (short*)nullptr, (short*)nullptr,
+                           (unsigned long long*)nullptr);
         hipLaunchKernelGGL(gemm_ws128, dim3(4, 16, 2), dim3(256), 0, stream,
                            Xh, Xl, Wh, Wl, P, 64);
         hipLaunchKernelGGL(reduce_feats_split, dim3(1072), dim3(256), 0, stream,
```

Result: slower. 253.3 us (+2.0%).
